# Optimization experiments

Hardware: AMD Instinct MI355X
Metric: run time of the kernel (lower is better)

## Reference

```python
import jax, jax.numpy as jnp
import numpy as np

# dims (match init_kwargs)
B, T, F = 2048, 252, 64      # batch, n_timestep, n_feature
C, L, K = 64, 4, 3           # channels, num levels, kernel_size
NOUT, NSEL = 500, 20         # n_output assets, n_select
LB, UB = 0.0, 0.1            # simplex box bounds
N_REBAL_ITERS = 16           # fixed bound on the water-filling loop (converges in a few iters)


def setup_inputs() -> dict:
    key = jax.random.key(0)
    ks = jax.random.split(key, 12)
    inp = {
        'x': jax.random.normal(ks[0], (B, T, F), dtype=jnp.float32),
        # TemporalBlock convs: init_weights() uses N(0, 0.01); weight_norm is a
        # reparametrization, so the effective conv weight is just a dense tensor.
        'conv1_w': 0.01 * jax.random.normal(ks[1], (L, C, C, K), dtype=jnp.float32),
        'conv1_b': 0.01 * jax.random.normal(ks[2], (L, C), dtype=jnp.float32),
        'conv2_w': 0.01 * jax.random.normal(ks[3], (L, C, C, K), dtype=jnp.float32),
        'conv2_b': 0.01 * jax.random.normal(ks[4], (L, C), dtype=jnp.float32),
        'proj_w': 0.05 * jax.random.normal(ks[5], (C, C), dtype=jnp.float32),
        'proj_b': 0.01 * jax.random.normal(ks[6], (C,), dtype=jnp.float32),
        'attn_w': 0.05 * jax.random.normal(ks[7], (NOUT, C), dtype=jnp.float32),
        'attn_b': 0.01 * jax.random.normal(ks[8], (NOUT,), dtype=jnp.float32),
        'fc_w': 0.05 * jax.random.normal(ks[9], (NOUT, C), dtype=jnp.float32),
        'fc_b': 0.01 * jax.random.normal(ks[10], (NOUT,), dtype=jnp.float32),
    }
    return inp


def _causal_conv(h, w, b, dil):
    # h: [B,C,T], w: [O,I,K]. torch pads both sides by (K-1)*dil then Chomp1d
    # removes the right pad -> equivalent to pure left (causal) padding.
    k = w.shape[-1]
    out = jax.lax.conv_general_dilated(
        h, w, window_strides=(1,), padding=[((k - 1) * dil, 0)],
        rhs_dilation=(dil,), dimension_numbers=('NCH', 'OIH', 'NCH'))
    return out + b[None, :, None]


def _rebalance(w, lb, ub, n_iters=N_REBAL_ITERS):
    # batched water-filling on the box-bounded simplex; mirrors the torch
    # do-while: redistribute clamped-off mass proportionally to non-capped weights.
    def step(old, wc):
        leftover = jnp.sum(old - wc)
        m = wc != ub
        nsum = jnp.sum(jnp.where(m, wc, 0.0))
        nsum = jnp.where(nsum == 0.0, 1.0, nsum)  # guard degenerate all-capped case
        return jnp.where(m, wc + leftover * wc / nsum, wc)

    cur = step(w, jnp.clip(w, lb, ub))           # first iteration (do-while)
    done0 = ~jnp.any(cur > ub)

    def body(carry, _):
        cur, done = carry
        nxt = step(cur, jnp.clip(cur, lb, ub))
        new = jnp.where(done, cur, nxt)
        return (new, done | ~jnp.any(new > ub)), None

    (res, _), _ = jax.lax.scan(body, (cur, done0), None, length=n_iters)
    return res


def reference(x, conv1_w, conv1_b, conv2_w, conv2_b,
              proj_w, proj_b, attn_w, attn_b, fc_w, fc_b):
    h = jnp.transpose(x, (0, 2, 1))  # [B,F,T]
    for i in range(L):  # fixed small loop over levels (structurally distinct dilations)
        d = 2 ** i
        o = jax.nn.relu(_causal_conv(h, conv1_w[i], conv1_b[i], d))
        o = jax.nn.relu(_causal_conv(o, conv2_w[i], conv2_b[i], d))
        h = jax.nn.relu(o + h)  # in==out channels -> identity residual
    pooled = jnp.max(h, axis=2)                       # MaxPool1d(T) + squeeze -> [B,C]
    z = jax.nn.relu(pooled @ proj_w.T + proj_b)       # proj (dropout=eval no-op)
    attn = jax.nn.sigmoid(z @ attn_w.T + attn_b)      # [B,NOUT]
    _, idx = jax.lax.top_k(attn, NSEL)
    mask = jnp.zeros_like(attn).at[jnp.arange(attn.shape[0])[:, None], idx].set(1.0)
    out = jax.nn.softmax(z @ fc_w.T + fc_b, axis=1) * mask
    out = out / (jnp.sum(out, axis=1, keepdims=True) + 1e-8)
    out = jax.vmap(lambda w: _rebalance(w, LB, UB))(out)
    return out
```

## Files before the change

### kernel.cpp

```cpp
#include <hip/hip_runtime.h>
#include <hip/hip_bf16.h>

#define T 252
#define NOUT 500
#define NSEL 20
#define UBV 0.1f

#define ROWS 272
#define PLANE_U (ROWS * 32)
#define LDS_BYTES (2 * PLANE_U * 4)

#define OFF_AWT    98304
#define OFF_FWT    130304
#define OFF_POOLED 162304

typedef short bf8 __attribute__((ext_vector_type(8)));
typedef float f32x4 __attribute__((ext_vector_type(4)));

static __device__ __forceinline__ unsigned short f2bf(float f) {
    unsigned u = __float_as_uint(f);
    return (unsigned short)((u + 0x7fffu + ((u >> 16) & 1u)) >> 16);
}
static __device__ __forceinline__ float bf2f(unsigned short h) {
    return __uint_as_float(((unsigned)h) << 16);
}
static __device__ __forceinline__ unsigned pk2bf(float a, float b) {
    __hip_bfloat162 h = __float22bfloat162_rn(float2{a, b});
    unsigned u; __builtin_memcpy(&u, &h, 4); return u;
}
static __device__ __forceinline__ float bf_lo_f(unsigned u) { return __uint_as_float(u << 16); }
static __device__ __forceinline__ float bf_hi_f(unsigned u) { return __uint_as_float(u & 0xffff0000u); }
static __device__ __forceinline__ int swz(int row, int chunk) {
    return row * 32 + ((chunk ^ (row & 7)) << 2);
}

__global__ __launch_bounds__(256) void prep_kernel(
    const float* __restrict__ w1, const float* __restrict__ w2,
    const float* __restrict__ aw, const float* __restrict__ fw,
    float* __restrict__ ws)
{
    int gid = blockIdx.x * 256 + threadIdx.x;
    if (gid < 24576) {
        int frag = gid >> 6, lane = gid & 63;
        int s   = frag & 1;
        int m   = (frag >> 1) & 3;
        int t3  = frag >> 3;
        int tap = t3 % 3;
        int q   = t3 / 3;
        int Kt  = q & 1;
        int lvl = (q >> 1) & 3;
        int buf = q >> 3;
        int c  = m * 16 + (lane & 15);
        int i0 = Kt * 32 + (lane >> 4) * 8;
        const float* W = (buf ? w2 : w1) + lvl * 12288 + c * 192;
        unsigned short v[8];
        for (int j = 0; j < 8; ++j) {
            float x = W[(i0 + j) * 3 + tap];
            unsigned short hi = f2bf(x);
            if (s == 0) v[j] = hi;
            else        v[j] = f2bf(x - bf2f(hi));
        }
        unsigned* dst = (unsigned*)ws + frag * 256 + lane * 4;
        for (int d = 0; d < 4; ++d)
            dst[d] = (unsigned)v[2 * d] | ((unsigned)v[2 * d + 1] << 16);
    }
    if (gid < 32000) {
        int a = gid >> 6, c = gid & 63;
        ws[OFF_AWT + c * 500 + a] = aw[gid];
        ws[OFF_FWT + c * 500 + a] = fw[gid];
    }
}

extern __shared__ unsigned short lds[];

#define MFMA(A, B, C) __builtin_amdgcn_mfma_f32_16x16x32_bf16((A), (B), (C), 0, 0, 0)

__global__ __launch_bounds__(256, 2) void conv_kernel(
    const float* __restrict__ x,
    const float* __restrict__ ws,
    const float* __restrict__ b1,
    const float* __restrict__ b2,
    float* __restrict__ pooled)
{
    const int b    = blockIdx.x;
    const int tid  = threadIdx.x;
    const int lane = tid & 63;
    const int wv   = tid >> 6;

    unsigned* Lh = (unsigned*)lds;
    unsigned* Ll = Lh + PLANE_U;

    for (int j = tid; j < 640; j += 256) {
        int r20 = j >> 5, col = j & 31;
        int r = (r20 < 16) ? r20 : (252 + r20);
        Lh[r * 32 + col] = 0u;
        Ll[r * 32 + col] = 0u;
    }
    const float4* xb = (const float4*)(x + (size_t)b * (T * 64));
    for (int v = tid; v < T * 16; v += 256) {
        float4 xv = xb[v];
        int t = v >> 4, f4 = v & 15;
        unsigned h01 = pk2bf(xv.x, xv.y);
        unsigned h23 = pk2bf(xv.z, xv.w);
        unsigned l01 = pk2bf(xv.x - bf_lo_f(h01), xv.y - bf_hi_f(h01));
        unsigned l23 = pk2bf(xv.z - bf_lo_f(h23), xv.w - bf_hi_f(h23));
        int row = 16 + t;
        int ui = swz(row, f4 >> 1) + ((f4 & 1) << 1);
        Lh[ui]     = h01;
        Lh[ui + 1] = h23;
        Ll[ui]     = l01;
        Ll[ui + 1] = l23;
    }
    __syncthreads();

    const uint4* AF4 = (const uint4*)ws;
    const int g    = lane >> 4;
    const int g4   = g << 2;
    const int ln16 = lane & 15;

    uint2 hh[4][4], hl[4][4];

    for (int lvl = 0; lvl < 4; ++lvl) {
        const int d = 1 << lvl;
        for (int cv = 0; cv < 2; ++cv) {
            const float* bias = (cv ? b2 : b1) + lvl * 64;
            f32x4 acc[4][4];
            #pragma unroll
            for (int m = 0; m < 4; ++m) {
                float4 bv = *(const float4*)(bias + m * 16 + g4);
                #pragma unroll
                for (int nn = 0; nn < 4; ++nn)
                    acc[m][nn] = (f32x4){bv.x, bv.y, bv.z, bv.w};
            }

            #pragma unroll
            for (int Kt = 0; Kt < 2; ++Kt) {
                #pragma unroll
                for (int tap = 0; tap < 3; ++tap) {
                    const int shift = (2 - tap) * d;
                    const int fb = (((cv * 4 + lvl) * 2 + Kt) * 3 + tap) * 8;
                    bf8 Bh[4], Bl[4];
                    #pragma unroll
                    for (int nn = 0; nn < 4; ++nn) {
                        int row = 16 + (4 * wv + nn) * 16 + ln16 - shift;
                        int ui  = swz(row, Kt * 4 + g);
                        Bh[nn] = *(const bf8*)(Lh + ui);
                        Bl[nn] = *(const bf8*)(Ll + ui);
                    }
                    #pragma unroll
                    for (int m = 0; m < 4; ++m) {
                        uint4 ta = AF4[(fb + 2 * m) * 64 + lane];
                        uint4 tb = AF4[(fb + 2 * m + 1) * 64 + lane];
                        bf8 Ah = *(bf8*)&ta;
                        bf8 Al = *(bf8*)&tb;
                        #pragma unroll
                        for (int nn = 0; nn < 4; ++nn) {
                            f32x4 a = acc[m][nn];
                            a = MFMA(Ah, Bh[nn], a);
                            a = MFMA(Ah, Bl[nn], a);
                            a = MFMA(Al, Bh[nn], a);
                            acc[m][nn] = a;
                        }
                    }
                }
            }

            if (cv == 0) {
                #pragma unroll
                for (int m = 0; m < 4; ++m)
                    #pragma unroll
                    for (int nn = 0; nn < 4; ++nn) {
                        int row = 16 + (4 * wv + nn) * 16 + ln16;
                        int cd  = m * 8 + (g4 >> 1);
                        int ui  = swz(row, cd >> 2) + (cd & 3);
                        hh[m][nn] = *(uint2*)(Lh + ui);
                        hl[m][nn] = *(uint2*)(Ll + ui);
                    }
                __syncthreads();
                #pragma unroll
                for (int m = 0; m < 4; ++m) {
                    #pragma unroll
                    for (int nn = 0; nn < 4; ++nn) {
                        int row = 16 + (4 * wv + nn) * 16 + ln16;
                        int cd  = m * 8 + (g4 >> 1);
                        int ui  = swz(row, cd >> 2) + (cd & 3);
                        float o0 = fmaxf(acc[m][nn][0], 0.f);
                        float o1 = fmaxf(acc[m][nn][1], 0.f);
                        float o2 = fmaxf(acc[m][nn][2], 0.f);
                        float o3 = fmaxf(acc[m][nn][3], 0.f);
                        uint2 wh, wl;
                        wh.x = pk2bf(o0, o1);
                        wh.y = pk2bf(o2, o3);
                        wl.x = pk2bf(o0 - bf_lo_f(wh.x), o1 - bf_hi_f(wh.x));
                        wl.y = pk2bf(o2 - bf_lo_f(wh.y), o3 - bf_hi_f(wh.y));
                        *(uint2*)(Lh + ui) = wh;
                        *(uint2*)(Ll + ui) = wl;
                    }
                }
                __syncthreads();
            } else {
                __syncthreads();
                #pragma unroll
                for (int m = 0; m < 4; ++m) {
                    #pragma unroll
                    for (int nn = 0; nn < 4; ++nn) {
                        int row = 16 + (4 * wv + nn) * 16 + ln16;
                        int cd  = m * 8 + (g4 >> 1);
                        int ui  = swz(row, cd >> 2) + (cd & 3);
                        float hold0 = bf_lo_f(hh[m][nn].x) + bf_lo_f(hl[m][nn].x);
                        float hold1 = bf_hi_f(hh[m][nn].x) + bf_hi_f(hl[m][nn].x);
                        float hold2 = bf_lo_f(hh[m][nn].y) + bf_lo_f(hl[m][nn].y);
                        float hold3 = bf_hi_f(hh[m][nn].y) + bf_hi_f(hl[m][nn].y);
                        float h0 = fmaxf(fmaxf(acc[m][nn][0], 0.f) + hold0, 0.f);
                        float h1 = fmaxf(fmaxf(acc[m][nn][1], 0.f) + hold1, 0.f);
                        float h2 = fmaxf(fmaxf(acc[m][nn][2], 0.f) + hold2, 0.f);
                        float h3 = fmaxf(fmaxf(acc[m][nn][3], 0.f) + hold3, 0.f);
                        uint2 wh, wl;
                        wh.x = pk2bf(h0, h1);
                        wh.y = pk2bf(h2, h3);
                        wl.x = pk2bf(h0 - bf_lo_f(wh.x), h1 - bf_hi_f(wh.x));
                        wl.y = pk2bf(h2 - bf_lo_f(wh.y), h3 - bf_hi_f(wh.y));
                        *(uint2*)(Lh + ui) = wh;
                        *(uint2*)(Ll + ui) = wl;
                    }
                }
                __syncthreads();
            }
        }
    }

    {
        int c = tid & 63, part = tid >> 6;
        int cd = c >> 1;
        float mx = 0.f;
        for (int j = 0; j < 63; ++j) {
            int row = 16 + part * 63 + j;
            int ui = swz(row, cd >> 2) + (cd & 3);
            int us = 2 * ui + (c & 1);
            mx = fmaxf(mx, bf2f(lds[us]) + bf2f(lds[2 * PLANE_U + us]));
        }
        __syncthreads();
        ((float*)lds)[tid] = mx;
        __syncthreads();
        if (tid < 64) {
            float* fs = (float*)lds;
            float mm = fmaxf(fmaxf(fs[tid], fs[tid + 64]),
                             fmaxf(fs[tid + 128], fs[tid + 192]));
            pooled[(size_t)b * 64 + tid] = mm;
        }
    }
}

__global__ __launch_bounds__(256) void head_kernel(
    const float* __restrict__ ws,
    const float* __restrict__ proj_w,
    const float* __restrict__ proj_b,
    const float* __restrict__ attn_b,
    const float* __restrict__ fc_b,
    float* __restrict__ out)
{
    const float* awT    = ws + OFF_AWT;
    const float* fwT    = ws + OFF_FWT;
    const float* pooled = ws + OFF_POOLED;

    __shared__ float z[64];
    __shared__ float att[512];
    __shared__ float pa[512];
    __shared__ int   msk[512];
    __shared__ float rs[4];

    const int b   = blockIdx.x;
    const int tid = threadIdx.x;
    const int wv  = tid >> 6, ln = tid & 63;

    if (tid < 64) {
        float s = proj_b[tid];
        const float* pw = proj_w + tid * 64;
        const float* pl = pooled + (size_t)b * 64;
        #pragma unroll 8
        for (int c = 0; c < 64; ++c) s = fmaf(pw[c], pl[c], s);
        z[tid] = fmaxf(s, 0.f);
    }
    __syncthreads();

    const int a0  = tid;
    const int a1  = tid + 256;
    const int a1e = (a1 < NOUT) ? a1 : (NOUT - 1);

    float l0 = attn_b[a0], l1 = attn_b[a1e];
    float f0 = fc_b[a0],   f1 = fc_b[a1e];
    #pragma unroll 8
    for (int c = 0; c < 64; ++c) {
        float zc = z[c];
        l0 = fmaf(zc, awT[c * 500 + a0],  l0);
        l1 = fmaf(zc, awT[c * 500 + a1e], l1);
        f0 = fmaf(zc, fwT[c * 500 + a0],  f0);
        f1 = fmaf(zc, fwT[c * 500 + a1e], f1);
    }
    float v0 = 1.f / (1.f + expf(-l0));
    float v1 = (a1 < NOUT) ? 1.f / (1.f + expf(-l1)) : 0.f;
    if (a1 >= NOUT) f1 = -1e30f;
    att[a0] = v0; att[a1] = v1;
    msk[a0] = 0;  msk[a1] = 0;
    __syncthreads();

    int selidx = 0;
    if (wv == 0) {
        float va[8];
        #pragma unroll
        for (int j = 0; j < 8; ++j) {
            int id = j * 64 + ln;
            va[j] = (id < NOUT) ? att[id] : 0.f;
        }
        for (int s = 0; s < NSEL; ++s) {
            float bv = va[0]; int bj = 0;
            #pragma unroll
            for (int j = 1; j < 8; ++j)
                if (va[j] > bv) { bv = va[j]; bj = j; }
            unsigned long long k =
                ((unsigned long long)__float_as_uint(bv) << 32)
                | (unsigned)(0xFFFFFFFFu - (unsigned)(bj * 64 + ln));
            for (int o = 32; o > 0; o >>= 1) {
                unsigned long long other = __shfl_xor(k, o);
                if (other > k) k = other;
            }
            int widx = (int)(0xFFFFFFFFu - (unsigned)(k & 0xFFFFFFFFu));
            if (ln == s) selidx = widx;
            if ((widx & 63) == ln) va[widx >> 6] = 0.f;
            if (ln == 0) msk[widx] = 1;
        }
    }
    __syncthreads();

    float mx = fmaxf(f0, f1);
    for (int o = 32; o > 0; o >>= 1) mx = fmaxf(mx, __shfl_xor(mx, o));
    if (ln == 0) rs[wv] = mx;
    __syncthreads();
    mx = fmaxf(fmaxf(rs[0], rs[1]), fmaxf(rs[2], rs[3]));
    __syncthreads();
    float e0 = expf(f0 - mx);
    float e1 = (a1 < NOUT) ? expf(f1 - mx) : 0.f;
    float sm = e0 + e1;
    for (int o = 32; o > 0; o >>= 1) sm += __shfl_xor(sm, o);
    if (ln == 0) rs[wv] = sm;
    __syncthreads();
    float Z = rs[0] + rs[1] + rs[2] + rs[3];

    float p0 = msk[a0] ? (e0 / Z) : 0.f;
    float p1 = (a1 < NOUT && msk[a1]) ? (e1 / Z) : 0.f;
    pa[a0] = p0; pa[a1] = p1;
    __syncthreads();

    if (wv == 0) {
        float w = (ln < NSEL) ? pa[selidx] : 0.f;
        float S = w;
        for (int o = 32; o > 0; o >>= 1) S += __shfl_xor(S, o);
        w = w / (S + 1e-8f);
        for (int it = 0; it < 17; ++it) {
            float wc = fminf(fmaxf(w, 0.f), UBV);
            float lo = w - wc;
            float ns = (wc != UBV) ? wc : 0.f;
            for (int o = 32; o > 0; o >>= 1) {
                lo += __shfl_xor(lo, o);
                ns += __shfl_xor(ns, o);
            }
            if (ns == 0.f) ns = 1.f;
            w = (wc != UBV) ? wc + lo * wc / ns : wc;
        }
        if (ln < NSEL) out[(size_t)b * NOUT + selidx] = w;
    }
    if (!msk[a0]) out[(size_t)b * NOUT + a0] = 0.f;
    if (a1 < NOUT && !msk[a1]) out[(size_t)b * NOUT + a1] = 0.f;
}

extern "C" void kernel_launch(void* const* d_in, const int* in_sizes, int n_in,
                              void* d_out, int out_size, void* d_ws, size_t ws_size,
                              hipStream_t stream)
{
    const float* x   = (const float*)d_in[0];
    const float* c1w = (const float*)d_in[1];
    const float* c1b = (const float*)d_in[2];
    const float* c2w = (const float*)d_in[3];
    const float* c2b = (const float*)d_in[4];
    const float* pw  = (const float*)d_in[5];
    const float* pb  = (const float*)d_in[6];
    const float* aw  = (const float*)d_in[7];
    const float* ab  = (const float*)d_in[8];
    const float* fw  = (const float*)d_in[9];
    const float* fb  = (const float*)d_in[10];

    float* ws  = (float*)d_ws;
    float* out = (float*)d_out;

    (void)hipFuncSetAttribute((const void*)conv_kernel,
                              hipFuncAttributeMaxDynamicSharedMemorySize,
                              LDS_BYTES);

    prep_kernel<<<128, 256, 0, stream>>>(c1w, c2w, aw, fw, ws);
    conv_kernel<<<2048, 256, LDS_BYTES, stream>>>(x, ws, c1b, c2b, ws + OFF_POOLED);
    head_kernel<<<2048, 256, 0, stream>>>(ws, pw, pb, ab, fb, out);
}
```

Baseline: 528.7 us.

## Keep residual in fp32 registers, pool from registers, split head projection across threads

The residual stream h now stays in fp32 registers for the whole conv stack instead of being re-read from the split bf16 LDS planes before each level. The final max-pool reduces from registers with a 16-lane shuffle, replacing a serial 63-row LDS scan. Conv inner loops are factored into a helper that hoists weight loads and precomputes swizzled addresses. The head projection is spread across all 256 threads with a shuffle reduction instead of a 64-thread serial dot product. Holding the residual in registers (64 floats per thread) adds register pressure, which could lower occupancy at launch_bounds(256,2).

```diff
diff --git a/kernel.cpp b/kernel.cpp
--- a/kernel.cpp
+++ b/kernel.cpp
@@ -75,6 +75,55 @@
 
 #define MFMA(A, B, C) __builtin_amdgcn_mfma_f32_16x16x32_bf16((A), (B), (C), 0, 0, 0)
 
+static __device__ __forceinline__ void conv_mm(
+    const uint4* __restrict__ AF4,
+    const unsigned* __restrict__ Lh, const unsigned* __restrict__ Ll,
+    const float* __restrict__ bias,
+    int cvlvl, int d, int Rb, int g, int g4, int lane,
+    f32x4 acc[4][4])
+{
+    #pragma unroll
+    for (int m = 0; m < 4; ++m) {
+        float4 bv = *(const float4*)(bias + m * 16 + g4);
+        #pragma unroll
+        for (int nn = 0; nn < 4; ++nn)
+            acc[m][nn] = (f32x4){bv.x, bv.y, bv.z, bv.w};
+    }
+    #pragma unroll
+    for (int Kt = 0; Kt < 2; ++Kt) {
+        #pragma unroll
+        for (int tap = 0; tap < 3; ++tap) {
+            const int fb = ((cvlvl * 2 + Kt) * 3 + tap) * 8;
+            const uint4* af = AF4 + fb * 64 + lane;
+            uint4 ta[4], tb[4];
+            #pragma unroll
+            for (int m = 0; m < 4; ++m) { ta[m] = af[m * 128]; tb[m] = af[m * 128 + 64]; }
+            const int shift = (2 - tap) * d;
+            const int row0  = Rb - shift;
+            const int ui0   = row0 * 32 + ((((Kt << 2) + g) ^ (row0 & 7)) << 2);
+            bf8 Bh[4], Bl[4];
+            #pragma unroll
+            for (int nn = 0; nn < 4; ++nn) {
+                Bh[nn] = *(const bf8*)(Lh + ui0 + nn * 512);
+                Bl[nn] = *(const bf8*)(Ll + ui0 + nn * 512);
+            }
+            #pragma unroll
+            for (int m = 0; m < 4; ++m) {
+                bf8 Ah = *(bf8*)&ta[m];
+                bf8 Al = *(bf8*)&tb[m];
+                #pragma unroll
+                for (int nn = 0; nn < 4; ++nn) {
+                    f32x4 a = acc[m][nn];
+                    a = MFMA(Ah, Bh[nn], a);
+                    a = MFMA(Ah, Bl[nn], a);
+                    a = MFMA(Al, Bh[nn], a);
+                    acc[m][nn] = a;
+                }
+            }
+        }
+    }
+}
+
 __global__ __launch_bounds__(256, 2) void conv_kernel(
     const float* __restrict__ x,
     const float* __restrict__ ws,
@@ -111,141 +160,122 @@
         Ll[ui]     = l01;
         Ll[ui + 1] = l23;
     }
-    __syncthreads();
-
-    const uint4* AF4 = (const uint4*)ws;
+
     const int g    = lane >> 4;
     const int g4   = g << 2;
     const int ln16 = lane & 15;
-
-    uint2 hh[4][4], hl[4][4];
+    const int Rb   = 16 + 64 * wv + ln16;
+
+    float hr[4][4][4];
+    #pragma unroll
+    for (int m = 0; m < 4; ++m)
+        #pragma unroll
+        for (int nn = 0; nn < 4; ++nn) {
+            int t = 64 * wv + 16 * nn + ln16;
+            if (t < T) {
+                float4 v = xb[t * 16 + m * 4 + g];
+                hr[m][nn][0] = v.x; hr[m][nn][1] = v.y;
+                hr[m][nn][2] = v.z; hr[m][nn][3] = v.w;
+            } else {
+                hr[m][nn][0] = 0.f; hr[m][nn][1] = 0.f;
+                hr[m][nn][2] = 0.f; hr[m][nn][3] = 0.f;
+            }
+        }
+    __syncthreads();
+
+    const uint4* AF4 = (const uint4*)ws;
+
+    int ue[4];
+    #pragma unroll
+    for (int m = 0; m < 4; ++m)
+        ue[m] = Rb * 32 + (((2 * m + (g >> 1)) ^ (Rb & 7)) << 2) + ((g & 1) << 1);
 
     for (int lvl = 0; lvl < 4; ++lvl) {
         const int d = 1 << lvl;
-        for (int cv = 0; cv < 2; ++cv) {
-            const float* bias = (cv ? b2 : b1) + lvl * 64;
-            f32x4 acc[4][4];
-            #pragma unroll
-            for (int m = 0; m < 4; ++m) {
-                float4 bv = *(const float4*)(bias + m * 16 + g4);
+        f32x4 acc[4][4];
+
+        conv_mm(AF4, Lh, Ll, b1 + lvl * 64, 0 * 4 + lvl, d, Rb, g, g4, lane, acc);
+        __syncthreads();
+        #pragma unroll
+        for (int m = 0; m < 4; ++m)
+            #pragma unroll
+            for (int nn = 0; nn < 4; ++nn) {
+                float o0 = fmaxf(acc[m][nn][0], 0.f);
+                float o1 = fmaxf(acc[m][nn][1], 0.f);
+                float o2 = fmaxf(acc[m][nn][2], 0.f);
+                float o3 = fmaxf(acc[m][nn][3], 0.f);
+                uint2 wh, wl;
+                wh.x = pk2bf(o0, o1);
+                wh.y = pk2bf(o2, o3);
+                wl.x = pk2bf(o0 - bf_lo_f(wh.x), o1 - bf_hi_f(wh.x));
+                wl.y = pk2bf(o2 - bf_lo_f(wh.y), o3 - bf_hi_f(wh.y));
+                int ui = ue[m] + nn * 512;
+                *(uint2*)(Lh + ui) = wh;
+                *(uint2*)(Ll + ui) = wl;
+            }
+        __syncthreads();
+
+        conv_mm(AF4, Lh, Ll, b2 + lvl * 64, 1 * 4 + lvl, d, Rb, g, g4, lane, acc);
+        #pragma unroll
+        for (int m = 0; m < 4; ++m)
+            #pragma unroll
+            for (int nn = 0; nn < 4; ++nn)
                 #pragma unroll
-                for (int nn = 0; nn < 4; ++nn)
-                    acc[m][nn] = (f32x4){bv.x, bv.y, bv.z, bv.w};
-            }
-
-            #pragma unroll
-            for (int Kt = 0; Kt < 2; ++Kt) {
+                for (int j = 0; j < 4; ++j)
+                    hr[m][nn][j] = fmaxf(fmaxf(acc[m][nn][j], 0.f) + hr[m][nn][j], 0.f);
+
+        if (lvl < 3) {
+            __syncthreads();
+            #pragma unroll
+            for (int m = 0; m < 4; ++m)
                 #pragma unroll
-                for (int tap = 0; tap < 3; ++tap) {
-                    const int shift = (2 - tap) * d;
-                    const int fb = (((cv * 4 + lvl) * 2 + Kt) * 3 + tap) * 8;
-                    bf8 Bh[4], Bl[4];
-                    #pragma unroll
-                    for (int nn = 0; nn < 4; ++nn) {
-                        int row = 16 + (4 * wv + nn) * 16 + ln16 - shift;
-                        int ui  = swz(row, Kt * 4 + g);
-                        Bh[nn] = *(const bf8*)(Lh + ui);
-                        Bl[nn] = *(const bf8*)(Ll + ui);
-                    }
-                    #pragma unroll
-                    for (int m = 0; m < 4; ++m) {
-                        uint4 ta = AF4[(fb + 2 * m) * 64 + lane];
-                        uint4 tb = AF4[(fb + 2 * m + 1) * 64 + lane];
-                        bf8 Ah = *(bf8*)&ta;
-                        bf8 Al = *(bf8*)&tb;
-                        #pragma unroll
-                        for (int nn = 0; nn < 4; ++nn) {
-                            f32x4 a = acc[m][nn];
-                            a = MFMA(Ah, Bh[nn], a);
-                            a = MFMA(Ah, Bl[nn], a);
-                            a = MFMA(Al, Bh[nn], a);
-                            acc[m][nn] = a;
-                        }
-                    }
+                for (int nn = 0; nn < 4; ++nn) {
+                    float h0 = hr[m][nn][0], h1 = hr[m][nn][1];
+                    float h2 = hr[m][nn][2], h3 = hr[m][nn][3];
+                    uint2 wh, wl;
+                    wh.x = pk2bf(h0, h1);
+                    wh.y = pk2bf(h2, h3);
+                    wl.x = pk2bf(h0 - bf_lo_f(wh.x), h1 - bf_hi_f(wh.x));
+                    wl.y = pk2bf(h2 - bf_lo_f(wh.y), h3 - bf_hi_f(wh.y));
+                    int ui = ue[m] + nn * 512;
+                    *(uint2*)(Lh + ui) = wh;
+                    *(uint2*)(Ll + ui) = wl;
                 }
-            }
-
-            if (cv == 0) {
+            __syncthreads();
+        }
+    }
+
+    __syncthreads();
+    {
+        const bool t3ok = (64 * wv + 48 + ln16) < T;
+        float pm[4][4];
+        #pragma unroll
+        for (int m = 0; m < 4; ++m)
+            #pragma unroll
+            for (int j = 0; j < 4; ++j) {
+                float p = fmaxf(fmaxf(hr[m][0][j], hr[m][1][j]), hr[m][2][j]);
+                if (t3ok) p = fmaxf(p, hr[m][3][j]);
+                pm[m][j] = p;
+            }
+        #pragma unroll
+        for (int off = 1; off < 16; off <<= 1)
+            #pragma unroll
+            for (int m = 0; m < 4; ++m)
                 #pragma unroll
-                for (int m = 0; m < 4; ++m)
-                    #pragma unroll
-                    for (int nn = 0; nn < 4; ++nn) {
-                        int row = 16 + (4 * wv + nn) * 16 + ln16;
-                        int cd  = m * 8 + (g4 >> 1);
-                        int ui  = swz(row, cd >> 2) + (cd & 3);
-                        hh[m][nn] = *(uint2*)(Lh + ui);
-                        hl[m][nn] = *(uint2*)(Ll + ui);
-                    }
-                __syncthreads();
+                for (int j = 0; j < 4; ++j)
+                    pm[m][j] = fmaxf(pm[m][j], __shfl_xor(pm[m][j], off));
+        float* fp = (float*)lds;
+        if (ln16 == 0) {
+            #pragma unroll
+            for (int m = 0; m < 4; ++m)
                 #pragma unroll
-                for (int m = 0; m < 4; ++m) {
-                    #pragma unroll
-                    for (int nn = 0; nn < 4; ++nn) {
-                        int row = 16 + (4 * wv + nn) * 16 + ln16;
-                        int cd  = m * 8 + (g4 >> 1);
-                        int ui  = swz(row, cd >> 2) + (cd & 3);
-                        float o0 = fmaxf(acc[m][nn][0], 0.f);
-                        float o1 = fmaxf(acc[m][nn][1], 0.f);
-                        float o2 = fmaxf(acc[m][nn][2], 0.f);
-                        float o3 = fmaxf(acc[m][nn][3], 0.f);
-                        uint2 wh, wl;
-                        wh.x = pk2bf(o0, o1);
-                        wh.y = pk2bf(o2, o3);
-                        wl.x = pk2bf(o0 - bf_lo_f(wh.x), o1 - bf_hi_f(wh.x));
-                        wl.y = pk2bf(o2 - bf_lo_f(wh.y), o3 - bf_hi_f(wh.y));
-                        *(uint2*)(Lh + ui) = wh;
-                        *(uint2*)(Ll + ui) = wl;
-                    }
-                }
-                __syncthreads();
-            } else {
-                __syncthreads();
-                #pragma unroll
-                for (int m = 0; m < 4; ++m) {
-                    #pragma unroll
-                    for (int nn = 0; nn < 4; ++nn) {
-                        int row = 16 + (4 * wv + nn) * 16 + ln16;
-                        int cd  = m * 8 + (g4 >> 1);
-                        int ui  = swz(row, cd >> 2) + (cd & 3);
-                        float hold0 = bf_lo_f(hh[m][nn].x) + bf_lo_f(hl[m][nn].x);
-                        float hold1 = bf_hi_f(hh[m][nn].x) + bf_hi_f(hl[m][nn].x);
-                        float hold2 = bf_lo_f(hh[m][nn].y) + bf_lo_f(hl[m][nn].y);
-                        float hold3 = bf_hi_f(hh[m][nn].y) + bf_hi_f(hl[m][nn].y);
-                        float h0 = fmaxf(fmaxf(acc[m][nn][0], 0.f) + hold0, 0.f);
-                        float h1 = fmaxf(fmaxf(acc[m][nn][1], 0.f) + hold1, 0.f);
-                        float h2 = fmaxf(fmaxf(acc[m][nn][2], 0.f) + hold2, 0.f);
-                        float h3 = fmaxf(fmaxf(acc[m][nn][3], 0.f) + hold3, 0.f);
-                        uint2 wh, wl;
-                        wh.x = pk2bf(h0, h1);
-                        wh.y = pk2bf(h2, h3);
-                        wl.x = pk2bf(h0 - bf_lo_f(wh.x), h1 - bf_hi_f(wh.x));
-                        wl.y = pk2bf(h2 - bf_lo_f(wh.y), h3 - bf_hi_f(wh.y));
-                        *(uint2*)(Lh + ui) = wh;
-                        *(uint2*)(Ll + ui) = wl;
-                    }
-                }
-                __syncthreads();
-            }
-        }
-    }
-
-    {
-        int c = tid & 63, part = tid >> 6;
-        int cd = c >> 1;
-        float mx = 0.f;
-        for (int j = 0; j < 63; ++j) {
-            int row = 16 + part * 63 + j;
-            int ui = swz(row, cd >> 2) + (cd & 3);
-            int us = 2 * ui + (c & 1);
-            mx = fmaxf(mx, bf2f(lds[us]) + bf2f(lds[2 * PLANE_U + us]));
-        }
-        __syncthreads();
-        ((float*)lds)[tid] = mx;
+                for (int j = 0; j < 4; ++j)
+                    fp[wv * 64 + m * 16 + g4 + j] = pm[m][j];
+        }
         __syncthreads();
         if (tid < 64) {
-            float* fs = (float*)lds;
-            float mm = fmaxf(fmaxf(fs[tid], fs[tid + 64]),
-                             fmaxf(fs[tid + 128], fs[tid + 192]));
+            float mm = fmaxf(fmaxf(fp[tid], fp[tid + 64]),
+                             fmaxf(fp[tid + 128], fp[tid + 192]));
             pooled[(size_t)b * 64 + tid] = mm;
         }
     }
@@ -273,13 +303,16 @@
     const int tid = threadIdx.x;
     const int wv  = tid >> 6, ln = tid & 63;
 
-    if (tid < 64) {
-        float s = proj_b[tid];
-        const float* pw = proj_w + tid * 64;
-        const float* pl = pooled + (size_t)b * 64;
-        #pragma unroll 8
-        for (int c = 0; c < 64; ++c) s = fmaf(pw[c], pl[c], s);
-        z[tid] = fmaxf(s, 0.f);
+    {
+        const int outc = tid >> 2, part = tid & 3;
+        const float* pw = proj_w + outc * 64 + part * 16;
+        const float* pl = pooled + (size_t)b * 64 + part * 16;
+        float s = 0.f;
+        #pragma unroll
+        for (int c = 0; c < 16; ++c) s = fmaf(pw[c], pl[c], s);
+        s += __shfl_xor(s, 1);
+        s += __shfl_xor(s, 2);
+        if (part == 0) z[outc] = fmaxf(s + proj_b[outc], 0.f);
     }
     __syncthreads();
 
```

New measurement: 510.7 us. -3.4%, faster.
